# Kernel tuning notes

Hardware: AMD Instinct MI355X
Metric: run time of the kernel (lower is better)

Reference implementation:

```python
import jax, jax.numpy as jnp
import numpy as np

D = 64       # CNF state dimension
H = 512      # MLP hidden width
B = 8192     # batch


def setup_inputs() -> dict:
    key = jax.random.key(0)
    ks = jax.random.split(key, 8)
    s1 = 1.0 / np.sqrt(D + 1)
    s2 = 1.0 / np.sqrt(H)
    return {
        "t": jax.random.uniform(ks[0], (1,), dtype=jnp.float32),
        "x": jax.random.normal(ks[1], (B, D + 1), dtype=jnp.float32),
        "W1": jax.random.normal(ks[2], (D + 1, H), dtype=jnp.float32) * s1,
        "b1": jnp.zeros((H,), dtype=jnp.float32),
        "W2": jax.random.normal(ks[3], (H, H), dtype=jnp.float32) * s2,
        "b2": jnp.zeros((H,), dtype=jnp.float32),
        "W3": jax.random.normal(ks[4], (H, D), dtype=jnp.float32) * s2,
        "b3": jnp.zeros((D,), dtype=jnp.float32),
    }


def reference(t, x, W1, b1, W2, b2, W3, b3):
    # CNF.forward: strip log-density channel, evaluate vf and its exact divergence.
    xs = x[..., :-1]                      # [B, D]
    tt = t[0]

    def vf_single(xi):                    # xi: [D] -> [D]
        inp = jnp.concatenate([tt[None], xi])          # vf(t*ones, x) with t prepended
        h = jnp.tanh(inp @ W1 + b1)
        h = jnp.tanh(h @ W2 + b2)
        return h @ W3 + b3

    dx = jax.vmap(vf_single)(xs)                        # [B, D]
    # exact divergence: trace of per-sample Jacobian via reverse-mode (matches torch jacrev)
    J = jax.vmap(jax.jacrev(vf_single))(xs)             # [B, D, D]
    div = jnp.trace(J, axis1=-2, axis2=-1)              # [B]
    return jnp.concatenate([dx, div[:, None]], axis=-1) # [B, D+1]
```

## Files before the change

kernel.cpp:

```cpp
#include <hip/hip_runtime.h>

#define HH 512
#define DD 64
#define MROWS 32
#define TPB 1024
#define LP 520

typedef unsigned short u16;
typedef short s16x8 __attribute__((ext_vector_type(8)));
typedef float f32x4 __attribute__((ext_vector_type(4)));

#define MFMA16(A,B,C) __builtin_amdgcn_mfma_f32_16x16x32_bf16((A),(B),(C),0,0,0)

#define OFF_EF   0
#define OFF_W2F  (HH*HH)
#define OFF_W1F  (2*HH*HH)
#define OFF_W3F  (2*HH*HH + HH*DD)
#define OFF_Z0B  ((2*HH*HH + 2*HH*DD)*2)

__device__ __forceinline__ u16 f2bf(float f) {
    unsigned u = __builtin_bit_cast(unsigned, f);
    u += 0x7fffu + ((u >> 16) & 1u);
    return (u16)(u >> 16);
}
__device__ __forceinline__ float bf2f(u16 h) {
    return __builtin_bit_cast(float, (unsigned)h << 16);
}
__device__ __forceinline__ float fast_tanh(float x) {
    float e = __expf(2.0f * x);
    return 1.0f - 2.0f * __builtin_amdgcn_rcpf(e + 1.0f);
}

__global__ __launch_bounds__(256) void precompute(
    const float* __restrict__ t,  const float* __restrict__ W1,
    const float* __restrict__ b1, const float* __restrict__ W2,
    const float* __restrict__ W3, u16* __restrict__ ws16, float* __restrict__ z0)
{
    __shared__ float T[16 * 264 > 256 * 20 ? 16 * 264 : 256 * 20];
    u16* Ef  = ws16 + OFF_EF;
    u16* W2f = ws16 + OFF_W2F;
    u16* W1f = ws16 + OFF_W1F;
    u16* W3f = ws16 + OFF_W3F;

    const int bid = blockIdx.x, tid = threadIdx.x;
    const int lane = tid & 63, wv = tid >> 6;
    const int m16 = lane & 15, q = lane >> 4;

    if (bid < 64) {
        const int nt = bid >> 1, bh = bid & 1;
        const int a0 = nt * 16, b0 = bh * 256;
        s16x8 afh[2], afl[2];
#pragma unroll
        for (int h = 0; h < 2; ++h)
#pragma unroll
            for (int j = 0; j < 8; ++j) {
                int i = h * 32 + q * 8 + j;
                float v = W1[(1 + i) * HH + a0 + m16];
                u16 hi = f2bf(v);
                afh[h][j] = (short)hi;
                afl[h][j] = (short)f2bf(v - bf2f(hi));
            }
#pragma unroll
        for (int bt = 0; bt < 4; ++bt) {
            int bl = wv * 64 + bt * 16;
            s16x8 bfh[2], bfl[2];
#pragma unroll
            for (int h = 0; h < 2; ++h) {
                const float* src = W3 + (b0 + bl + m16) * DD + h * 32 + q * 8;
                float4 p0 = *(const float4*)(src);
                float4 p1 = *(const float4*)(src + 4);
                float vv[8] = {p0.x,p0.y,p0.z,p0.w,p1.x,p1.y,p1.z,p1.w};
#pragma unroll
                for (int j = 0; j < 8; ++j) {
                    u16 hi = f2bf(vv[j]);
                    bfh[h][j] = (short)hi;
                    bfl[h][j] = (short)f2bf(vv[j] - bf2f(hi));
                }
            }
            f32x4 c = {0.f, 0.f, 0.f, 0.f};
#pragma unroll
            for (int h = 0; h < 2; ++h) {
                c = MFMA16(afh[h], bfh[h], c);
                c = MFMA16(afh[h], bfl[h], c);
                c = MFMA16(afl[h], bfh[h], c);
            }
#pragma unroll
            for (int r = 0; r < 4; ++r)
                T[(4 * q + r) * 264 + bl + m16] = c[r];
        }
        __syncthreads();
#pragma unroll
        for (int p = 0; p < 2; ++p) {
            int ksl = p * 4 + wv;
            int al  = m16;
            int blc = ksl * 32 + q * 8;
            const float* w2p = W2 + (a0 + al) * HH + b0 + blc;
            float4 wa = *(const float4*)(w2p), wb = *(const float4*)(w2p + 4);
            const float* glp = T + al * 264 + blc;
            s16x8 o;
            o[0]=(short)f2bf(wa.x*glp[0]); o[1]=(short)f2bf(wa.y*glp[1]);
            o[2]=(short)f2bf(wa.z*glp[2]); o[3]=(short)f2bf(wa.w*glp[3]);
            o[4]=(short)f2bf(wb.x*glp[4]); o[5]=(short)f2bf(wb.y*glp[5]);
            o[6]=(short)f2bf(wb.z*glp[6]); o[7]=(short)f2bf(wb.w*glp[7]);
            *(s16x8*)(Ef + nt * 8192 + (b0 / 32 + ksl) * 512 + lane * 8) = o;
        }
        if (bh == 0 && tid < 128) {
            int ks = tid >> 6, ln = tid & 63;
            int n  = nt * 16 + (ln & 15);
            int k0 = ks * 32 + (ln >> 4) * 8;
            s16x8 o;
#pragma unroll
            for (int j = 0; j < 8; ++j) o[j] = (short)f2bf(W1[(1 + k0 + j) * HH + n]);
            *(s16x8*)(W1f + nt * 1024 + ks * 512 + ln * 8) = o;
        }
    } else if (bid < 128) {
        const int nt = (bid - 64) >> 1, kh = (bid - 64) & 1;
        const int n0 = nt * 16, k0 = kh * 256;
#pragma unroll
        for (int it = 0; it < 4; ++it) {
            int r = (tid >> 2) + it * 64;
            int c = (tid & 3) * 4;
            float4 v = *(const float4*)(W2 + (k0 + r) * HH + n0 + c);
            *(float4*)(T + r * 20 + c) = v;
        }
        __syncthreads();
#pragma unroll
        for (int p = 0; p < 2; ++p) {
            int ksl = p * 4 + wv;
            int kq  = ksl * 32 + q * 8;
            s16x8 o;
#pragma unroll
            for (int j = 0; j < 8; ++j) o[j] = (short)f2bf(T[(kq + j) * 20 + m16]);
            *(s16x8*)(W2f + nt * 8192 + (k0 / 32 + ksl) * 512 + lane * 8) = o;
        }
    } else if (bid < 136) {
        const int ot = (bid - 128) >> 1, kh = (bid - 128) & 1;
        const int o0 = ot * 16, k0 = kh * 256;
#pragma unroll
        for (int it = 0; it < 4; ++it) {
            int r = (tid >> 2) + it * 64;
            int c = (tid & 3) * 4;
            float4 v = *(const float4*)(W3 + (k0 + r) * DD + o0 + c);
            *(float4*)(T + r * 20 + c) = v;
        }
        __syncthreads();
#pragma unroll
        for (int p = 0; p < 2; ++p) {
            int ksl = p * 4 + wv;
            int kq  = ksl * 32 + q * 8;
            s16x8 o;
#pragma unroll
            for (int j = 0; j < 8; ++j) o[j] = (short)f2bf(T[(kq + j) * 20 + m16]);
            *(s16x8*)(W3f + ot * 8192 + (k0 / 32 + ksl) * 512 + lane * 8) = o;
        }
    } else {
        for (int n = tid; n < HH; n += 256)
            z0[n] = b1[n] + t[0] * W1[n];
    }
}

__global__ __launch_bounds__(TPB) void cnf_main(
    const float* __restrict__ x,  const u16* __restrict__ ws16,
    const float* __restrict__ z0, const float* __restrict__ b2,
    const float* __restrict__ b3, float* __restrict__ out)
{
    __shared__ u16 h1s[MROWS * LP];
    __shared__ u16 h2s[MROWS * LP];
    __shared__ u16 d2s[MROWS * LP];
    __shared__ float z0s[HH];
    __shared__ float b2s[HH];
    __shared__ float b3s[DD];
    __shared__ float divacc[16][MROWS];

    const u16* Ef  = ws16 + OFF_EF;
    const u16* W2f = ws16 + OFF_W2F;
    const u16* W1f = ws16 + OFF_W1F;
    const u16* W3f = ws16 + OFF_W3F;

    const int tid  = threadIdx.x;
    const int lane = tid & 63;
    const int w    = tid >> 6;
    const int m16  = lane & 15;
    const int q    = lane >> 4;
    const int kq   = q * 8;
    const int r0   = blockIdx.x * MROWS;

    const int noff = (blockIdx.x >> 3) & 31;
    const int koff = (blockIdx.x >> 3) & 15;

    const int tile0 = (2 * w + noff) & 31;
    const int tile1 = (2 * w + 1 + noff) & 31;
    const int col0  = tile0 * 16 + m16;
    const int col1  = tile1 * 16 + m16;

    u16* xs = d2s;

    s16x8 p1b[2][2];
    {
        const u16* bb0 = W1f + tile0 * 1024 + lane * 8;
        const u16* bb1 = W1f + tile1 * 1024 + lane * 8;
        p1b[0][0] = *(const s16x8*)(bb0);
        p1b[0][1] = *(const s16x8*)(bb0 + 512);
        p1b[1][0] = *(const s16x8*)(bb1);
        p1b[1][1] = *(const s16x8*)(bb1 + 512);
    }
    const u16* w2bp0 = W2f + tile0 * 8192 + lane * 8;
    const u16* w2bp1 = W2f + tile1 * 8192 + lane * 8;
    s16x8 B0[4], B1[4];
#pragma unroll
    for (int k = 0; k < 4; ++k) {
        const int kk = (koff + k) & 15;
        B0[k] = *(const s16x8*)(w2bp0 + kk * 512);
        B1[k] = *(const s16x8*)(w2bp1 + kk * 512);
    }

    for (int idx = tid; idx < MROWS * DD; idx += TPB) {
        int r = idx >> 6, c = idx & 63;
        xs[r * 72 + c] = f2bf(x[(r0 + r) * (DD + 1) + c]);
    }
    if (tid < HH) { z0s[tid] = z0[tid]; b2s[tid] = b2[tid]; }
    if (tid < DD) b3s[tid] = b3[tid];
    __syncthreads();

    float d1reg[2][2][4];

    {
        s16x8 xa[2][2];
#pragma unroll
        for (int rt = 0; rt < 2; ++rt)
#pragma unroll
            for (int h = 0; h < 2; ++h)
                xa[rt][h] = *(const s16x8*)(xs + (rt * 16 + m16) * 72 + h * 32 + kq);
#pragma unroll
        for (int ct = 0; ct < 2; ++ct) {
            int col = ct ? col1 : col0;
#pragma unroll
            for (int rt = 0; rt < 2; ++rt) {
                f32x4 c = {0.f, 0.f, 0.f, 0.f};
                c = MFMA16(xa[rt][0], p1b[ct][0], c);
                c = MFMA16(xa[rt][1], p1b[ct][1], c);
#pragma unroll
                for (int i = 0; i < 4; ++i) {
                    float hv = fast_tanh(c[i] + z0s[col]);
                    h1s[(rt * 16 + 4 * q + i) * LP + col] = f2bf(hv);
                    d1reg[rt][ct][i] = 1.0f - hv * hv;
                }
            }
        }
    }
    __syncthreads();

    f32x4 a00={0,0,0,0}, a01={0,0,0,0}, a10={0,0,0,0}, a11={0,0,0,0};
    {
        const u16* ap0 = h1s + m16 * LP + kq;
        const u16* ap1 = h1s + (16 + m16) * LP + kq;
#pragma unroll
        for (int ks = 0; ks < 16; ++ks) {
            const int kk = (koff + ks) & 15;
            s16x8 f0 = *(const s16x8*)(ap0 + kk * 32);
            s16x8 f1 = *(const s16x8*)(ap1 + kk * 32);
            const int sl = ks & 3;
            a00 = MFMA16(f0, B0[sl], a00);
            a10 = MFMA16(f1, B0[sl], a10);
            a01 = MFMA16(f0, B1[sl], a01);
            a11 = MFMA16(f1, B1[sl], a11);
            if (ks < 12) {
                const int kn = (koff + ks + 4) & 15;
                B0[sl] = *(const s16x8*)(w2bp0 + kn * 512);
                B1[sl] = *(const s16x8*)(w2bp1 + kn * 512);
            }
        }
    }

    const u16* efp0 = Ef + tile0 * 8192 + lane * 8;
    const u16* efp1 = Ef + tile1 * 8192 + lane * 8;
    s16x8 E0[4], E1[4];
#pragma unroll
    for (int k = 0; k < 2; ++k) {
        const int kk = (koff + k) & 15;
        E0[k] = *(const s16x8*)(efp0 + kk * 512);
        E1[k] = *(const s16x8*)(efp1 + kk * 512);
    }

    {
        f32x4 acc[2][2] = {{a00, a01}, {a10, a11}};
#pragma unroll
        for (int rt = 0; rt < 2; ++rt)
#pragma unroll
            for (int ct = 0; ct < 2; ++ct) {
                int col = ct ? col1 : col0;
#pragma unroll
                for (int i = 0; i < 4; ++i) {
                    int row = rt * 16 + 4 * q + i;
                    float hv = fast_tanh(acc[rt][ct][i] + b2s[col]);
                    h2s[row * LP + col] = f2bf(hv);
                    d2s[row * LP + col] = f2bf(1.0f - hv * hv);
                }
            }
    }
    __syncthreads();

    if (w < 8) {
        const int rowt = w >> 2;
        const int ot   = (w + noff) & 3;
        const u16* ap = h2s + (rowt * 16 + m16) * LP + kq;
        const u16* bp = W3f + ot * 8192 + lane * 8;
        s16x8 W3r[4];
#pragma unroll
        for (int k = 0; k < 4; ++k)
            W3r[k] = *(const s16x8*)(bp + ((koff + k) & 15) * 512);
        f32x4 cA = {0.f,0.f,0.f,0.f}, cB = {0.f,0.f,0.f,0.f};
#pragma unroll
        for (int ks = 0; ks < 16; ++ks) {
            const int kk = (koff + ks) & 15;
            s16x8 f = *(const s16x8*)(ap + kk * 32);
            const int sl = ks & 3;
            if (ks & 1) cB = MFMA16(f, W3r[sl], cB);
            else        cA = MFMA16(f, W3r[sl], cA);
            if (ks < 12) W3r[sl] = *(const s16x8*)(bp + ((koff + ks + 4) & 15) * 512);
        }
        f32x4 c3 = cA + cB;
        int o = ot * 16 + m16;
#pragma unroll
        for (int i = 0; i < 4; ++i)
            out[(r0 + rowt * 16 + 4 * q + i) * (DD + 1) + o] = c3[i] + b3s[o];
    }

    {
        f32x4 g00={0,0,0,0}, g01={0,0,0,0}, g10={0,0,0,0}, g11={0,0,0,0};
        const u16* ap0 = d2s + m16 * LP + kq;
        const u16* ap1 = d2s + (16 + m16) * LP + kq;
#pragma unroll
        for (int ks = 0; ks < 16; ++ks) {
            const int kk = (koff + ks) & 15;
            s16x8 f0 = *(const s16x8*)(ap0 + kk * 32);
            s16x8 f1 = *(const s16x8*)(ap1 + kk * 32);
            const int sl = ks & 3;
            g00 = MFMA16(f0, E0[sl], g00);
            g10 = MFMA16(f1, E0[sl], g10);
            g01 = MFMA16(f0, E1[sl], g01);
            g11 = MFMA16(f1, E1[sl], g11);
            if (ks < 14) {
                const int dl = (ks + 2) & 3;
                const int kn = (koff + ks + 2) & 15;
                E0[dl] = *(const s16x8*)(efp0 + kn * 512);
                E1[dl] = *(const s16x8*)(efp1 + kn * 512);
            }
        }
        f32x4 acc[2][2] = {{g00, g01}, {g10, g11}};
#pragma unroll
        for (int rt = 0; rt < 2; ++rt)
#pragma unroll
            for (int i = 0; i < 4; ++i) {
                float v = d1reg[rt][0][i] * acc[rt][0][i]
                        + d1reg[rt][1][i] * acc[rt][1][i];
                v += __shfl_xor(v, 1, 64);
                v += __shfl_xor(v, 2, 64);
                v += __shfl_xor(v, 4, 64);
                v += __shfl_xor(v, 8, 64);
                if (m16 == 0) divacc[w][rt * 16 + 4 * q + i] = v;
            }
    }
    __syncthreads();

    if (tid < MROWS) {
        float s = 0.0f;
#pragma unroll
        for (int ww = 0; ww < 16; ++ww) s += divacc[ww][tid];
        out[(r0 + tid) * (DD + 1) + DD] = s;
    }
}

extern "C" void kernel_launch(void* const* d_in, const int* in_sizes, int n_in,
                              void* d_out, int out_size, void* d_ws, size_t ws_size,
                              hipStream_t stream) {
    const float* t  = (const float*)d_in[0];
    const float* x  = (const float*)d_in[1];
    const float* W1 = (const float*)d_in[2];
    const float* b1 = (const float*)d_in[3];
    const float* W2 = (const float*)d_in[4];
    const float* b2 = (const float*)d_in[5];
    const float* W3 = (const float*)d_in[6];
    const float* b3 = (const float*)d_in[7];
    float* out = (float*)d_out;

    u16*   ws16 = (u16*)d_ws;
    float* z0   = (float*)((char*)d_ws + OFF_Z0B);

    precompute<<<137, 256, 0, stream>>>(t, W1, b1, W2, W3, ws16, z0);
    cnf_main<<<8192 / MROWS, TPB, 0, stream>>>(x, ws16, z0, b2, b3, out);
}
```

Measured before the change: 90.03 us.

## Halve block to 512 threads, give each wave four column tiles

Result: slower. 92.20 us (+2.4%).

```diff
diff --git a/kernel.cpp b/kernel.cpp
--- a/kernel.cpp
+++ b/kernel.cpp
@@ -3,7 +3,7 @@
 #define HH 512
 #define DD 64
 #define MROWS 32
-#define TPB 1024
+#define TPB 512
 #define LP 520
 
 typedef unsigned short u16;
@@ -159,7 +159,7 @@
     }
 }
 
-__global__ __launch_bounds__(TPB) void cnf_main(
+__global__ __launch_bounds__(TPB, 2) void cnf_main(
     const float* __restrict__ x,  const u16* __restrict__ ws16,
     const float* __restrict__ z0, const float* __restrict__ b2,
     const float* __restrict__ b3, float* __restrict__ out)
@@ -170,7 +170,7 @@
     __shared__ float z0s[HH];
     __shared__ float b2s[HH];
     __shared__ float b3s[DD];
-    __shared__ float divacc[16][MROWS];
+    __shared__ float divacc[8][MROWS];
 
     const u16* Ef  = ws16 + OFF_EF;
     const u16* W2f = ws16 + OFF_W2F;
@@ -188,30 +188,29 @@
     const int noff = (blockIdx.x >> 3) & 31;
     const int koff = (blockIdx.x >> 3) & 15;
 
-    const int tile0 = (2 * w + noff) & 31;
-    const int tile1 = (2 * w + 1 + noff) & 31;
-    const int col0  = tile0 * 16 + m16;
-    const int col1  = tile1 * 16 + m16;
+    int tile[4];
+#pragma unroll
+    for (int ct = 0; ct < 4; ++ct) tile[ct] = (4 * w + ct + noff) & 31;
 
     u16* xs = d2s;
 
-    s16x8 p1b[2][2];
-    {
-        const u16* bb0 = W1f + tile0 * 1024 + lane * 8;
-        const u16* bb1 = W1f + tile1 * 1024 + lane * 8;
-        p1b[0][0] = *(const s16x8*)(bb0);
-        p1b[0][1] = *(const s16x8*)(bb0 + 512);
-        p1b[1][0] = *(const s16x8*)(bb1);
-        p1b[1][1] = *(const s16x8*)(bb1 + 512);
-    }
-    const u16* w2bp0 = W2f + tile0 * 8192 + lane * 8;
-    const u16* w2bp1 = W2f + tile1 * 8192 + lane * 8;
-    s16x8 B0[4], B1[4];
+    s16x8 p1b[4][2];
+#pragma unroll
+    for (int ct = 0; ct < 4; ++ct) {
+        const u16* bb = W1f + tile[ct] * 1024 + lane * 8;
+        p1b[ct][0] = *(const s16x8*)(bb);
+        p1b[ct][1] = *(const s16x8*)(bb + 512);
+    }
+    const u16* w2bp[4];
+#pragma unroll
+    for (int ct = 0; ct < 4; ++ct) w2bp[ct] = W2f + tile[ct] * 8192 + lane * 8;
+    s16x8 Bv[4][4];
 #pragma unroll
     for (int k = 0; k < 4; ++k) {
         const int kk = (koff + k) & 15;
-        B0[k] = *(const s16x8*)(w2bp0 + kk * 512);
-        B1[k] = *(const s16x8*)(w2bp1 + kk * 512);
+#pragma unroll
+        for (int ct = 0; ct < 4; ++ct)
+            Bv[k][ct] = *(const s16x8*)(w2bp[ct] + kk * 512);
     }
 
     for (int idx = tid; idx < MROWS * DD; idx += TPB) {
@@ -222,7 +221,7 @@
     if (tid < DD) b3s[tid] = b3[tid];
     __syncthreads();
 
-    float d1reg[2][2][4];
+    float d1reg[2][4][4];
 
     {
         s16x8 xa[2][2];
@@ -232,8 +231,9 @@
             for (int h = 0; h < 2; ++h)
                 xa[rt][h] = *(const s16x8*)(xs + (rt * 16 + m16) * 72 + h * 32 + kq);
 #pragma unroll
-        for (int ct = 0; ct < 2; ++ct) {
-            int col = ct ? col1 : col0;
+        for (int ct = 0; ct < 4; ++ct) {
+            const int col = tile[ct] * 16 + m16;
+            const float zc = z0s[col];
 #pragma unroll
             for (int rt = 0; rt < 2; ++rt) {
                 f32x4 c = {0.f, 0.f, 0.f, 0.f};
@@ -241,7 +241,7 @@
                 c = MFMA16(xa[rt][1], p1b[ct][1], c);
 #pragma unroll
                 for (int i = 0; i < 4; ++i) {
-                    float hv = fast_tanh(c[i] + z0s[col]);
+                    float hv = fast_tanh(c[i] + zc);
                     h1s[(rt * 16 + 4 * q + i) * LP + col] = f2bf(hv);
                     d1reg[rt][ct][i] = 1.0f - hv * hv;
                 }
@@ -250,57 +250,71 @@
     }
     __syncthreads();
 
-    f32x4 a00={0,0,0,0}, a01={0,0,0,0}, a10={0,0,0,0}, a11={0,0,0,0};
+    f32x4 acc[2][4];
+#pragma unroll
+    for (int rt = 0; rt < 2; ++rt)
+#pragma unroll
+        for (int ct = 0; ct < 4; ++ct) acc[rt][ct] = (f32x4){0.f,0.f,0.f,0.f};
     {
         const u16* ap0 = h1s + m16 * LP + kq;
         const u16* ap1 = h1s + (16 + m16) * LP + kq;
+        s16x8 Aq[2][2];
+        {
+            const int kk0 = koff & 15;
+            Aq[0][0] = *(const s16x8*)(ap0 + kk0 * 32);
+            Aq[0][1] = *(const s16x8*)(ap1 + kk0 * 32);
+        }
 #pragma unroll
         for (int ks = 0; ks < 16; ++ks) {
-            const int kk = (koff + ks) & 15;
-            s16x8 f0 = *(const s16x8*)(ap0 + kk * 32);
-            s16x8 f1 = *(const s16x8*)(ap1 + kk * 32);
-            const int sl = ks & 3;
-            a00 = MFMA16(f0, B0[sl], a00);
-            a10 = MFMA16(f1, B0[sl], a10);
-            a01 = MFMA16(f0, B1[sl], a01);
-            a11 = MFMA16(f1, B1[sl], a11);
+            const int sl = ks & 3, cur = ks & 1;
+            if (ks < 15) {
+                const int kn = (koff + ks + 1) & 15;
+                Aq[cur ^ 1][0] = *(const s16x8*)(ap0 + kn * 32);
+                Aq[cur ^ 1][1] = *(const s16x8*)(ap1 + kn * 32);
+            }
+#pragma unroll
+            for (int ct = 0; ct < 4; ++ct) {
+                acc[0][ct] = MFMA16(Aq[cur][0], Bv[sl][ct], acc[0][ct]);
+                acc[1][ct] = MFMA16(Aq[cur][1], Bv[sl][ct], acc[1][ct]);
+            }
             if (ks < 12) {
                 const int kn = (koff + ks + 4) & 15;
-                B0[sl] = *(const s16x8*)(w2bp0 + kn * 512);
-                B1[sl] = *(const s16x8*)(w2bp1 + kn * 512);
-            }
-        }
-    }
-
-    const u16* efp0 = Ef + tile0 * 8192 + lane * 8;
-    const u16* efp1 = Ef + tile1 * 8192 + lane * 8;
-    s16x8 E0[4], E1[4];
+#pragma unroll
+                for (int ct = 0; ct < 4; ++ct)
+                    Bv[sl][ct] = *(const s16x8*)(w2bp[ct] + kn * 512);
+            }
+        }
+    }
+
+    const u16* efp[4];
+#pragma unroll
+    for (int ct = 0; ct < 4; ++ct) efp[ct] = Ef + tile[ct] * 8192 + lane * 8;
+    s16x8 Ev[4][4];
 #pragma unroll
     for (int k = 0; k < 2; ++k) {
         const int kk = (koff + k) & 15;
-        E0[k] = *(const s16x8*)(efp0 + kk * 512);
-        E1[k] = *(const s16x8*)(efp1 + kk * 512);
-    }
+#pragma unroll
+        for (int ct = 0; ct < 4; ++ct)
+            Ev[k][ct] = *(const s16x8*)(efp[ct] + kk * 512);
+    }
+
+#pragma unroll
+    for (int rt = 0; rt < 2; ++rt)
+#pragma unroll
+        for (int ct = 0; ct < 4; ++ct) {
+            const int col = tile[ct] * 16 + m16;
+            const float bc = b2s[col];
+#pragma unroll
+            for (int i = 0; i < 4; ++i) {
+                int row = rt * 16 + 4 * q + i;
+                float hv = fast_tanh(acc[rt][ct][i] + bc);
+                h2s[row * LP + col] = f2bf(hv);
+                d2s[row * LP + col] = f2bf(1.0f - hv * hv);
+            }
+        }
+    __syncthreads();
 
     {
-        f32x4 acc[2][2] = {{a00, a01}, {a10, a11}};
-#pragma unroll
-        for (int rt = 0; rt < 2; ++rt)
-#pragma unroll
-            for (int ct = 0; ct < 2; ++ct) {
-                int col = ct ? col1 : col0;
-#pragma unroll
-                for (int i = 0; i < 4; ++i) {
-                    int row = rt * 16 + 4 * q + i;
-                    float hv = fast_tanh(acc[rt][ct][i] + b2s[col]);
-                    h2s[row * LP + col] = f2bf(hv);
-                    d2s[row * LP + col] = f2bf(1.0f - hv * hv);
-                }
-            }
-    }
-    __syncthreads();
-
-    if (w < 8) {
         const int rowt = w >> 2;
         const int ot   = (w + noff) & 3;
         const u16* ap = h2s + (rowt * 16 + m16) * LP + kq;
@@ -320,40 +334,62 @@
             if (ks < 12) W3r[sl] = *(const s16x8*)(bp + ((koff + ks + 4) & 15) * 512);
         }
         f32x4 c3 = cA + cB;
-        int o = ot * 16 + m16;
+        const int o = ot * 16 + m16;
 #pragma unroll
         for (int i = 0; i < 4; ++i)
             out[(r0 + rowt * 16 + 4 * q + i) * (DD + 1) + o] = c3[i] + b3s[o];
     }
 
     {
-        f32x4 g00={0,0,0,0}, g01={0,0,0,0}, g10={0,0,0,0}, g11={0,0,0,0};
-        const u16* ap0 = d2s + m16 * LP + kq;
-        const u16* ap1 = d2s + (16 + m16) * LP + kq;
+        f32x4 g[2][4];
+#pragma unroll
+        for (int rt = 0; rt < 2; ++rt)
+#pragma unroll
+            for (int ct = 0; ct < 4; ++ct) g[rt][ct] = (f32x4){0.f,0.f,0.f,0.f};
+
+#pragma unroll
+        for (int k = 2; k < 4; ++k) {
+            const int kk = (koff + k) & 15;
+#pragma unroll
+            for (int ct = 0; ct < 4; ++ct)
+                Ev[k][ct] = *(const s16x8*)(efp[ct] + kk * 512);
+        }
+        const u16* dp0 = d2s + m16 * LP + kq;
+        const u16* dp1 = d2s + (16 + m16) * LP + kq;
+        s16x8 Aq[2][2];
+        {
+            const int kk0 = koff & 15;
+            Aq[0][0] = *(const s16x8*)(dp0 + kk0 * 32);
+            Aq[0][1] = *(const s16x8*)(dp1 + kk0 * 32);
+        }
 #pragma unroll
         for (int ks = 0; ks < 16; ++ks) {
-            const int kk = (koff + ks) & 15;
-            s16x8 f0 = *(const s16x8*)(ap0 + kk * 32);
-            s16x8 f1 = *(const s16x8*)(ap1 + kk * 32);
-            const int sl = ks & 3;
-            g00 = MFMA16(f0, E0[sl], g00);
-            g10 = MFMA16(f1, E0[sl], g10);
-            g01 = MFMA16(f0, E1[sl], g01);
-            g11 = MFMA16(f1, E1[sl], g11);
-            if (ks < 14) {
-                const int dl = (ks + 2) & 3;
-                const int kn = (koff + ks + 2) & 15;
-                E0[dl] = *(const s16x8*)(efp0 + kn * 512);
-                E1[dl] = *(const s16x8*)(efp1 + kn * 512);
-            }
-        }
-        f32x4 acc[2][2] = {{g00, g01}, {g10, g11}};
+            const int sl = ks & 3, cur = ks & 1;
+            if (ks < 15) {
+                const int kn = (koff + ks + 1) & 15;
+                Aq[cur ^ 1][0] = *(const s16x8*)(dp0 + kn * 32);
+                Aq[cur ^ 1][1] = *(const s16x8*)(dp1 + kn * 32);
+            }
+#pragma unroll
+            for (int ct = 0; ct < 4; ++ct) {
+                g[0][ct] = MFMA16(Aq[cur][0], Ev[sl][ct], g[0][ct]);
+                g[1][ct] = MFMA16(Aq[cur][1], Ev[sl][ct], g[1][ct]);
+            }
+            if (ks < 12) {
+                const int kn = (koff + ks + 4) & 15;
+#pragma unroll
+                for (int ct = 0; ct < 4; ++ct)
+                    Ev[sl][ct] = *(const s16x8*)(efp[ct] + kn * 512);
+            }
+        }
 #pragma unroll
         for (int rt = 0; rt < 2; ++rt)
 #pragma unroll
             for (int i = 0; i < 4; ++i) {
-                float v = d1reg[rt][0][i] * acc[rt][0][i]
-                        + d1reg[rt][1][i] * acc[rt][1][i];
+                float v = d1reg[rt][0][i] * g[rt][0][i]
+                        + d1reg[rt][1][i] * g[rt][1][i]
+                        + d1reg[rt][2][i] * g[rt][2][i]
+                        + d1reg[rt][3][i] * g[rt][3][i];
                 v += __shfl_xor(v, 1, 64);
                 v += __shfl_xor(v, 2, 64);
                 v += __shfl_xor(v, 4, 64);
@@ -366,7 +402,7 @@
     if (tid < MROWS) {
         float s = 0.0f;
 #pragma unroll
-        for (int ww = 0; ww < 16; ++ww) s += divacc[ww][tid];
+        for (int ww = 0; ww < 8; ++ww) s += divacc[ww][tid];
         out[(r0 + tid) * (DD + 1) + DD] = s;
     }
 }
```
